# Kernel tuning notes

Measured on AMD Instinct MI355X. Metric: run time of the kernel, lower is better.

The kernel has to match this reference:

```python
import jax, jax.numpy as jnp
import numpy as np

D_MODEL = 1024
N_HEAD = 16
HEAD_DIM = D_MODEL // N_HEAD
D_FF = int(D_MODEL * 4.0)
B, T = 2, 2048


def rms_norm(x, eps=1e-6):
    return x * jax.lax.rsqrt(jnp.mean(jnp.square(x), axis=-1, keepdims=True) + eps)


def rope_tables(T, head_dim):
    # half-truncated RoPE: first quarter of dims get real freqs, next quarter zeros
    angular_freq = (1.0 / 1024.0) ** jnp.linspace(0.0, 1.0, head_dim // 4, dtype=jnp.float32)
    angular_freq = jnp.concatenate([angular_freq, jnp.zeros(head_dim // 4, jnp.float32)])
    theta = jnp.arange(T, dtype=jnp.float32)[:, None] * angular_freq[None, :]  # [T, head_dim//2]
    return jnp.cos(theta), jnp.sin(theta)


def apply_rope(x, cos, sin):
    # x: [B, H, T, D]; cos/sin: [T, D//2]
    x1, x2 = jnp.split(x.astype(jnp.float32), 2, axis=-1)
    c = cos[None, None]
    s = sin[None, None]
    y1 = x1 * c + x2 * s
    y2 = -x1 * s + x2 * c
    return jnp.concatenate([y1, y2], axis=-1).astype(x.dtype)


def setup_inputs() -> dict:
    key = jax.random.key(0)
    ks = jax.random.split(key, 10)
    x = jax.random.normal(ks[0], (B, T, D_MODEL), jnp.float32)
    block_mask = jnp.tril(jnp.ones((T, T), jnp.bool_))  # causal
    sc = 1.0 / np.sqrt(D_MODEL)
    Wqkv = jax.random.normal(ks[1], (D_MODEL, 3 * D_MODEL), jnp.float32) * sc
    bqkv = jnp.zeros((3 * D_MODEL,), jnp.float32)
    Wo = jax.random.normal(ks[2], (D_MODEL, D_MODEL), jnp.float32) * sc
    bo = jnp.zeros((D_MODEL,), jnp.float32)
    W1 = jax.random.normal(ks[3], (D_MODEL, D_FF), jnp.float32) * sc
    b1 = jnp.zeros((D_FF,), jnp.float32)
    W2 = jax.random.normal(ks[4], (D_FF, D_MODEL), jnp.float32) * (1.0 / np.sqrt(D_FF))
    b2 = jnp.zeros((D_MODEL,), jnp.float32)
    return {"x": x, "block_mask": block_mask, "Wqkv": Wqkv, "bqkv": bqkv,
            "Wo": Wo, "bo": bo, "W1": W1, "b1": b1, "W2": W2, "b2": b2}


def reference(x, block_mask, Wqkv, bqkv, Wo, bo, W1, b1, W2, b2):
    Bq, Tq, D = x.shape
    cos, sin = rope_tables(Tq, HEAD_DIM)

    def attn(h):
        qkv = h @ Wqkv + bqkv  # [B, T, 3D]
        qkv = qkv.reshape(Bq, Tq, 3, N_HEAD, HEAD_DIM)
        qkv = jnp.transpose(qkv, (2, 0, 3, 1, 4))  # [3, B, H, T, d]
        q, k, v = qkv[0], qkv[1], qkv[2]
        q, k = rms_norm(q), rms_norm(k)
        q, k = apply_rope(q, cos, sin), apply_rope(k, cos, sin)
        scores = jnp.einsum('bhtd,bhsd->bhts', q, k) / np.sqrt(HEAD_DIM)
        scores = jnp.where(block_mask[None, None], scores, jnp.float32(-1e30))
        p = jax.nn.softmax(scores, axis=-1)
        o = jnp.einsum('bhts,bhsd->bhtd', p, v)
        o = jnp.transpose(o, (0, 2, 1, 3)).reshape(Bq, Tq, D)
        return o @ Wo + bo

    def mlp(h):
        return jax.nn.gelu(h @ W1 + b1) @ W2 + b2

    x = x + attn(rms_norm(x))
    x = x + mlp(rms_norm(x))
    return x
```

## Files before the change

### kernel.cpp

```cpp
#include <hip/hip_runtime.h>
#include <hip/hip_bf16.h>


typedef __attribute__((ext_vector_type(8))) short short8;
typedef __attribute__((ext_vector_type(4))) float f32x4;
typedef __attribute__((ext_vector_type(4))) unsigned short u16x4;
typedef __attribute__((ext_vector_type(8))) unsigned short u16x8;

#define MROWS 4096
#define DMODEL 1024
#define DFF 4096
#define NH 16
#define HD 64
#define SEQ 2048

static __device__ __forceinline__ unsigned short f2bf(float f) {
    union { __hip_bfloat16 b; unsigned short u; } cv;
    cv.b = __float2bfloat16(f);
    return cv.u;
}

static __device__ __forceinline__ void gload_lds16(const void* g, void* l) {
    __builtin_amdgcn_global_load_lds(
        (const __attribute__((address_space(1))) unsigned int*)g,
        (__attribute__((address_space(3))) unsigned int*)l, 16, 0, 0);
}

static __device__ __forceinline__ int xcd_swizzle(int id, int nwg) {
    const int nx = 8;
    const int q = nwg / nx, r = nwg % nx;
    const int xcd = id % nx, loc = id / nx;
    return (xcd < r ? xcd * (q + 1) : r * (q + 1) + (xcd - r) * q) + loc;
}

__global__ void cast_transpose(const float* __restrict__ W,
                               unsigned short* __restrict__ Wt, int K, int N) {
    __shared__ float tile[32][33];
    const int tx = threadIdx.x & 31;
    const int ty = threadIdx.x >> 5;
    const int n0 = blockIdx.x * 32, k0 = blockIdx.y * 32;
#pragma unroll
    for (int i = 0; i < 4; ++i) {
        int kk = ty + i * 8;
        tile[kk][tx] = W[(long)(k0 + kk) * N + n0 + tx];
    }
    __syncthreads();
#pragma unroll
    for (int i = 0; i < 4; ++i) {
        int nn = ty + i * 8;
        Wt[(long)(n0 + nn) * K + k0 + tx] = f2bf(tile[tx][nn]);
    }
}

__global__ void rope_table(float* __restrict__ cosT, float* __restrict__ sinT) {
    const int t = blockIdx.x, j = threadIdx.x;
    float th = (j < 16) ? (float)t * exp2f(-(10.0f / 15.0f) * (float)j) : 0.0f;
    cosT[t * 32 + j] = cosf(th);
    sinT[t * 32 + j] = sinf(th);
}

__global__ void rmsnorm_cast(const float* __restrict__ xin,
                             unsigned short* __restrict__ hout) {
    const int row = blockIdx.x;
    const float4 v = ((const float4*)(xin + (long)row * DMODEL))[threadIdx.x];
    float ss = v.x * v.x + v.y * v.y + v.z * v.z + v.w * v.w;
#pragma unroll
    for (int m = 32; m >= 1; m >>= 1) ss += __shfl_xor(ss, m);
    __shared__ float part[4];
    if ((threadIdx.x & 63) == 0) part[threadIdx.x >> 6] = ss;
    __syncthreads();
    const float tot = part[0] + part[1] + part[2] + part[3];
    const float sc = rsqrtf(tot * (1.0f / (float)DMODEL) + 1e-6f);
    ushort4 o;
    o.x = f2bf(v.x * sc); o.y = f2bf(v.y * sc);
    o.z = f2bf(v.z * sc); o.w = f2bf(v.w * sc);
    ((ushort4*)hout)[(long)row * (DMODEL / 4) + threadIdx.x] = o;
}

template <int EPI, int BN, int BK>
__launch_bounds__(256)
__global__ void gemm_bt(const short* __restrict__ A, const short* __restrict__ Bt,
                        const float* __restrict__ bias, const float* __restrict__ res,
                        float* __restrict__ outF, unsigned short* __restrict__ outB,
                        int N, int K) {
    constexpr int NF = BN / 32;
    constexpr int CPR = BK / 8;
    __shared__ short As[2][128 * BK];
    __shared__ short Bs[2][BN * BK];
    const int tid = threadIdx.x;
    const int lane = tid & 63, w = tid >> 6;
    const int wr = w >> 1, wc = w & 1;
    const int l16 = lane & 15, lhi = lane >> 4;

    const int nwg = gridDim.x * gridDim.y;
    int id = xcd_swizzle(blockIdx.y * gridDim.x + blockIdx.x, nwg);
    const int bx = id % gridDim.x, by = id / gridDim.x;
    const long rowA0 = (long)by * 128;
    const long rowB0 = (long)bx * BN;

    const f32x4 fz = {0.f, 0.f, 0.f, 0.f};
    f32x4 acc[4][NF];
#pragma unroll
    for (int m = 0; m < 4; ++m)
#pragma unroll
        for (int n = 0; n < NF; ++n) acc[m][n] = fz;

    auto stage = [&](int kt, int b) {
        const int k0 = kt * BK;
#pragma unroll
        for (int it = 0; it < BK / 16; ++it) {
            const int c = it * 256 + tid;
            const int r = c / CPR, col = (c % CPR) * 8;
            gload_lds16(A + (rowA0 + r) * K + k0 + col, (char*)As[b] + c * 16);
        }
#pragma unroll
        for (int it = 0; it < (BN * BK) / 2048; ++it) {
            const int c = it * 256 + tid;
            const int r = c / CPR, col = (c % CPR) * 8;
            gload_lds16(Bt + (rowB0 + r) * K + k0 + col, (char*)Bs[b] + c * 16);
        }
    };
    auto compute = [&](int b) {
#pragma unroll
        for (int kk = 0; kk < BK / 32; ++kk) {
            short8 af[4], bf[NF];
#pragma unroll
            for (int m = 0; m < 4; ++m)
                af[m] = *(const short8*)(&As[b][0] + (wr * 64 + m * 16 + l16) * BK + kk * 32 + lhi * 8);
#pragma unroll
            for (int n = 0; n < NF; ++n)
                bf[n] = *(const short8*)(&Bs[b][0] + (wc * (BN / 2) + n * 16 + l16) * BK + kk * 32 + lhi * 8);
#pragma unroll
            for (int m = 0; m < 4; ++m)
#pragma unroll
                for (int n = 0; n < NF; ++n)
                    acc[m][n] = __builtin_amdgcn_mfma_f32_16x16x32_bf16(
                        af[m], bf[n], acc[m][n], 0, 0, 0);
        }
    };

    const int ktiles = K / BK;
    stage(0, 0);
    __syncthreads();
    int cur = 0;
    for (int kt = 0; kt < ktiles; ++kt) {
        if (kt + 1 < ktiles) stage(kt + 1, cur ^ 1);
        compute(cur);
        __syncthreads();
        cur ^= 1;
    }

#pragma unroll
    for (int m = 0; m < 4; ++m) {
        const long r0 = rowA0 + wr * 64 + m * 16 + lhi * 4;
#pragma unroll
        for (int n = 0; n < NF; ++n) {
            const long cc = rowB0 + wc * (BN / 2) + n * 16 + l16;
            const float bv = bias[cc];
#pragma unroll
            for (int j = 0; j < 4; ++j) {
                const long idx = (r0 + j) * N + cc;
                float v = acc[m][n][j] + bv;
                if (EPI == 1) v += res[idx];
                if (EPI == 2) {
                    float g = 0.5f * v *
                        (1.0f + tanhf(0.7978845608028654f * (v + 0.044715f * v * v * v)));
                    outB[idx] = f2bf(g);
                } else {
                    outF[idx] = v;
                }
            }
        }
    }
}

__global__ void qkv_post(const float* __restrict__ qkv, const float* __restrict__ cosT,
                         const float* __restrict__ sinT, unsigned short* __restrict__ Qo,
                         unsigned short* __restrict__ Ko) {
    const int lane = threadIdx.x & 63;
    const int g = blockIdx.x * 4 + (threadIdx.x >> 6);
    const int row = g >> 4, h = g & 15;
    const int b = row >> 11, t = row & 2047;
    const float* base = qkv + (long)row * 3072 + h * 64;
    float q = base[lane];
    float k = base[1024 + lane];
    float sq = q * q, sk = k * k;
#pragma unroll
    for (int m = 32; m >= 1; m >>= 1) {
        sq += __shfl_xor(sq, m);
        sk += __shfl_xor(sk, m);
    }
    q *= rsqrtf(sq * (1.0f / 64.0f) + 1e-6f);
    k *= rsqrtf(sk * (1.0f / 64.0f) + 1e-6f);
    const int j = lane & 31;
    const float c = cosT[t * 32 + j], s = sinT[t * 32 + j];
    const float q2 = __shfl_xor(q, 32), k2 = __shfl_xor(k, 32);
    const float sgn = (lane < 32) ? 1.0f : -1.0f;
    const float qr = q * c + sgn * q2 * s;
    const float kr = k * c + sgn * k2 * s;
    const long o = ((long)(b * 16 + h) * SEQ + t) * 64 + lane;
    Qo[o] = f2bf(qr * 0.125f);
    Ko[o] = f2bf(kr);
}

__global__ void transpose_v(const float* __restrict__ qkv,
                            unsigned short* __restrict__ Vt) {
    __shared__ float tile[64][65];
    const int tid = threadIdx.x;
    const int bh = blockIdx.x, tt = blockIdx.y;
    const int b = bh >> 4, h = bh & 15;
    const int tr = tid >> 2, c0 = (tid & 3) * 16;
    const float* src = qkv + ((long)(b * SEQ + tt * 64 + tr)) * 3072 + 2048 + h * 64 + c0;
#pragma unroll
    for (int i = 0; i < 4; ++i) {
        float4 v = ((const float4*)src)[i];
        tile[tr][c0 + i * 4 + 0] = v.x;
        tile[tr][c0 + i * 4 + 1] = v.y;
        tile[tr][c0 + i * 4 + 2] = v.z;
        tile[tr][c0 + i * 4 + 3] = v.w;
    }
    __syncthreads();
    const int d = tid >> 2, t0 = (tid & 3) * 16;
    unsigned short* dst = Vt + ((long)bh * 64 + d) * SEQ + tt * 64 + t0;
#pragma unroll
    for (int half = 0; half < 2; ++half) {
        u16x8 o;
#pragma unroll
        for (int e = 0; e < 8; ++e) o[e] = f2bf(tile[t0 + half * 8 + e][d]);
        *(u16x8*)(dst + half * 8) = o;
    }
}

__launch_bounds__(256)
__global__ void attn_fwd(const short* __restrict__ Qg, const short* __restrict__ Kg,
                         const short* __restrict__ Vtg, unsigned short* __restrict__ Og) {
    __shared__ short Ks[2][64 * 64];
    __shared__ short Vs[2][64 * 64];
    __shared__ char Ps[4][2048];
    const int tid = threadIdx.x, lane = tid & 63, w = tid >> 6;
    const int l16 = lane & 15, lhi = lane >> 4;
    const int id = xcd_swizzle(blockIdx.y * gridDim.x + blockIdx.x, 512);
    const int bh = id >> 4;
    const int ip = id & 15;
    const int bb = bh >> 4, hh = bh & 15;
    const long base_q = (long)bh * (SEQ * 64);
    char* Pw = &Ps[w][0];
    const int swz = (l16 & 7) << 4;
    const f32x4 fz = {0.f, 0.f, 0.f, 0.f};

#pragma unroll 1
    for (int rep = 0; rep < 2; ++rep) {
        const int qt = rep ? ip : 31 - ip;
        short8 aq0, aq1;
        {
            const short* Qp = Qg + base_q + (long)(qt * 64 + w * 16) * 64;
            aq0 = *(const short8*)(Qp + l16 * 64 + lhi * 8);
            aq1 = *(const short8*)(Qp + l16 * 64 + 32 + lhi * 8);
        }
        float mrow = -1e30f, lrow = 0.f;
        f32x4 oacc[4];
#pragma unroll
        for (int n = 0; n < 4; ++n) oacc[n] = fz;

        auto stage = [&](int kt, int b) {
            const short* Kp = Kg + base_q + (long)kt * 64 * 64;
            const short* Vp = Vtg + base_q + (long)kt * 64;
#pragma unroll
            for (int it = 0; it < 2; ++it) {
                const int c = it * 256 + tid;
                const int r = c >> 3;
                const int col = ((c & 7) ^ (r & 7)) << 3;
                gload_lds16(Kp + r * 64 + col, (char*)&Ks[b][0] + c * 16);
                gload_lds16(Vp + (long)r * SEQ + col, (char*)&Vs[b][0] + c * 16);
            }
        };

        stage(0, 0);
        __syncthreads();
        int cur = 0;
        for (int kt = 0; kt <= qt; ++kt) {
            if (kt < qt) stage(kt + 1, cur ^ 1);
            const short* KsC = &Ks[cur][0];
            const short* VsC = &Vs[cur][0];

            f32x4 s[4];
            __builtin_amdgcn_s_setprio(1);
#pragma unroll
            for (int n = 0; n < 4; ++n) {
                const int kr = n * 16 + l16;
                short8 bk0 = *(const short8*)(KsC + kr * 64 + ((lhi ^ (kr & 7)) << 3));
                short8 bk1 = *(const short8*)(KsC + kr * 64 + (((lhi + 4) ^ (kr & 7)) << 3));
                f32x4 z = fz;
                z = __builtin_amdgcn_mfma_f32_16x16x32_bf16(bk0, aq0, z, 0, 0, 0);
                s[n] = __builtin_amdgcn_mfma_f32_16x16x32_bf16(bk1, aq1, z, 0, 0, 0);
            }
            __builtin_amdgcn_s_setprio(0);
            if (kt == qt) {
#pragma unroll
                for (int n = 0; n < 4; ++n)
#pragma unroll
                    for (int j = 0; j < 4; ++j)
                        if (n * 16 + lhi * 4 + j > w * 16 + l16) s[n][j] = -1e30f;
            }

            float pm = s[0][0];
#pragma unroll
            for (int n = 0; n < 4; ++n)
#pragma unroll
                for (int j = 0; j < 4; ++j) pm = fmaxf(pm, s[n][j]);
            pm = fmaxf(pm, __shfl_xor(pm, 16));
            pm = fmaxf(pm, __shfl_xor(pm, 32));
            if (!__all(pm <= mrow + 8.f)) {
                const float newm = fmaxf(mrow, pm);
                const float sc = __expf(mrow - newm);
                mrow = newm;
                lrow *= sc;
#pragma unroll
                for (int j = 0; j < 4; ++j) {
                    const float scj = __shfl(sc, lhi * 4 + j);
#pragma unroll
                    for (int n = 0; n < 4; ++n) oacc[n][j] *= scj;
                }
            }
            float ps = 0.f;
#pragma unroll
            for (int n = 0; n < 4; ++n)
#pragma unroll
                for (int j = 0; j < 4; ++j) {
                    const float p = __expf(s[n][j] - mrow);
                    s[n][j] = p;
                    ps += p;
                }
            ps += __shfl_xor(ps, 16);
            ps += __shfl_xor(ps, 32);
            lrow += ps;

#pragma unroll
            for (int n = 0; n < 4; ++n) {
                u16x4 pk;
                pk[0] = f2bf(s[n][0]);
                pk[1] = f2bf(s[n][1]);
                pk[2] = f2bf(s[n][2]);
                pk[3] = f2bf(s[n][3]);
                *(u16x4*)(Pw + ((l16 * 128 + n * 32 + lhi * 8) ^ swz)) = pk;
            }

            __builtin_amdgcn_s_setprio(1);
#pragma unroll
            for (int ks = 0; ks < 2; ++ks) {
                short8 pa = *(const short8*)(Pw + ((l16 * 128 + ks * 64 + lhi * 16) ^ swz));
#pragma unroll
                for (int n = 0; n < 4; ++n) {
                    const int dr = n * 16 + l16;
                    short8 vb = *(const short8*)(VsC + dr * 64 + ((((ks << 2) + lhi) ^ (dr & 7)) << 3));
                    oacc[n] = __builtin_amdgcn_mfma_f32_16x16x32_bf16(pa, vb, oacc[n], 0, 0, 0);
                }
            }
            __builtin_amdgcn_s_setprio(0);
            __syncthreads();
            cur ^= 1;
        }

#pragma unroll
        for (int j = 0; j < 4; ++j) {
            const float lr = __shfl(lrow, lhi * 4 + j);
            const int qrow = qt * 64 + w * 16 + lhi * 4 + j;
            const long orow = (long)bb * SEQ + qrow;
#pragma unroll
            for (int n = 0; n < 4; ++n)
                Og[orow * DMODEL + hh * 64 + n * 16 + l16] = f2bf(oacc[n][j] / lr);
        }
    }
}

extern "C" void kernel_launch(void* const* d_in, const int* in_sizes, int n_in,
                              void* d_out, int out_size, void* d_ws, size_t ws_size,
                              hipStream_t stream) {
    const float* x    = (const float*)d_in[0];
    const float* Wqkv = (const float*)d_in[2];
    const float* bqkv = (const float*)d_in[3];
    const float* Wo   = (const float*)d_in[4];
    const float* bo   = (const float*)d_in[5];
    const float* W1   = (const float*)d_in[6];
    const float* b1   = (const float*)d_in[7];
    const float* W2   = (const float*)d_in[8];
    const float* b2   = (const float*)d_in[9];
    float* out = (float*)d_out;

    char* ws = (char*)d_ws;
    auto alloc = [&](size_t b) {
        char* p = ws;
        ws += (b + 255) & ~(size_t)255;
        return p;
    };
    short* WqkvT = (short*)alloc(3072ull * 1024 * 2);
    short* WoT   = (short*)alloc(1024ull * 1024 * 2);
    short* W1T   = (short*)alloc(4096ull * 1024 * 2);
    short* W2T   = (short*)alloc(1024ull * 4096 * 2);
    float* cosT  = (float*)alloc(2048ull * 32 * 4);
    float* sinT  = (float*)alloc(2048ull * 32 * 4);
    short* hbuf  = (short*)alloc((size_t)MROWS * DMODEL * 2);
    short* Qb    = (short*)alloc(32ull * SEQ * 64 * 2);
    short* Kb    = (short*)alloc(32ull * SEQ * 64 * 2);
    short* Vtb   = (short*)alloc(32ull * 64 * SEQ * 2);
    short* Ob    = (short*)alloc((size_t)MROWS * DMODEL * 2);
    float* x1    = (float*)alloc((size_t)MROWS * DMODEL * 4);
    char*  big   = alloc((size_t)MROWS * 3072 * 4);
    float* qkv   = (float*)big;
    unsigned short* act = (unsigned short*)big;

    cast_transpose<<<dim3(96, 32), 256, 0, stream>>>(Wqkv, (unsigned short*)WqkvT, 1024, 3072);
    cast_transpose<<<dim3(32, 32), 256, 0, stream>>>(Wo, (unsigned short*)WoT, 1024, 1024);
    cast_transpose<<<dim3(128, 32), 256, 0, stream>>>(W1, (unsigned short*)W1T, 1024, 4096);
    cast_transpose<<<dim3(32, 128), 256, 0, stream>>>(W2, (unsigned short*)W2T, 4096, 1024);
    rope_table<<<2048, 32, 0, stream>>>(cosT, sinT);
    rmsnorm_cast<<<MROWS, 256, 0, stream>>>(x, (unsigned short*)hbuf);
    gemm_bt<0, 128, 32><<<dim3(24, 32), 256, 0, stream>>>(hbuf, WqkvT, bqkv, nullptr, qkv, nullptr, 3072, 1024);
    qkv_post<<<16384, 256, 0, stream>>>(qkv, cosT, sinT,
                                        (unsigned short*)Qb, (unsigned short*)Kb);
    transpose_v<<<dim3(32, 32), 256, 0, stream>>>(qkv, (unsigned short*)Vtb);
    attn_fwd<<<dim3(16, 32), 256, 0, stream>>>(Qb, Kb, Vtb, (unsigned short*)Ob);
    gemm_bt<1, 64, 64><<<dim3(16, 32), 256, 0, stream>>>(Ob, WoT, bo, x, x1, nullptr, 1024, 1024);
    rmsnorm_cast<<<MROWS, 256, 0, stream>>>(x1, (unsigned short*)hbuf);
    gemm_bt<2, 128, 32><<<dim3(32, 32), 256, 0, stream>>>(hbuf, W1T, b1, nullptr, nullptr, act, 4096, 1024);
    gemm_bt<1, 64, 64><<<dim3(16, 32), 256, 0, stream>>>((const short*)act, W2T, b2, x1, out, nullptr, 1024, 4096);
}
```

Before: 412.8 us.

## Add 256x256-tile 512-thread GEMM with 4-stage LDS pipeline for QKV and FFN1

Adds a new GEMM kernel that uses 256x256 output tiles, 8 waves per block and a four-buffer direct-to-LDS prefetch pipeline with swizzled LDS layout and explicit vmcnt waits. It replaces the 128-wide gemm_bt for the QKV projection and the first MLP matmul, aiming for more data reuse per loaded tile and better latency hiding. The larger tiles give far fewer workgroups (192 and 256), which may underfill the 256 CUs, and the 64 KB of LDS plus large accumulator arrays per block may limit occupancy.

```diff
diff --git a/kernel.cpp b/kernel.cpp
--- a/kernel.cpp
+++ b/kernel.cpp
@@ -75,6 +75,108 @@
     o.x = f2bf(v.x * sc); o.y = f2bf(v.y * sc);
     o.z = f2bf(v.z * sc); o.w = f2bf(v.w * sc);
     ((ushort4*)hout)[(long)row * (DMODEL / 4) + threadIdx.x] = o;
+}
+
+template <int EPI>
+__launch_bounds__(512, 2)
+__global__ void gemm256(const short* __restrict__ A, const short* __restrict__ Bt,
+                        const float* __restrict__ bias,
+                        float* __restrict__ outF, unsigned short* __restrict__ outB,
+                        int N, int K) {
+    __shared__ __align__(16) short As[4][128 * 64];
+    __shared__ __align__(16) short Bs[4][128 * 64];
+    const int tid = threadIdx.x;
+    const int lane = tid & 63, w = tid >> 6;
+    const int wr = w >> 2, wc = w & 3;
+    const int l16 = lane & 15, lhi = lane >> 4;
+
+    const int nwg = gridDim.x * gridDim.y;
+    int id = xcd_swizzle(blockIdx.y * gridDim.x + blockIdx.x, nwg);
+    const int bx = id % gridDim.x, by = id / gridDim.x;
+    const long rowA0 = (long)by * 256;
+    const long rowB0 = (long)bx * 256;
+
+    const f32x4 fz = {0.f, 0.f, 0.f, 0.f};
+    f32x4 acc[8][4];
+#pragma unroll
+    for (int m = 0; m < 8; ++m)
+#pragma unroll
+        for (int n = 0; n < 4; ++n) acc[m][n] = fz;
+
+    auto stage = [&](int kt, int b) {
+        const int k0 = kt << 5;
+#pragma unroll
+        for (int pass = 0; pass < 2; ++pass) {
+            const int c = pass * 512 + tid;
+            const int line = c >> 3, pch = c & 7;
+            const int lch = pch ^ (line & 7);
+            const int row = ((lch >> 2) << 7) + line;
+            const int kc = (lch & 3) << 3;
+            gload_lds16(A + (rowA0 + row) * K + k0 + kc, (char*)&As[b][0] + c * 16);
+            gload_lds16(Bt + (rowB0 + row) * K + k0 + kc, (char*)&Bs[b][0] + c * 16);
+        }
+    };
+    auto compute = [&](int b) {
+        const short* Ab = &As[b][0];
+        const short* Bb = &Bs[b][0];
+        short8 af[8], bf[4];
+#pragma unroll
+        for (int m = 0; m < 8; ++m) {
+            const int line = m * 16 + l16;
+            const int pch = ((wr << 2) + lhi) ^ (line & 7);
+            af[m] = *(const short8*)(Ab + line * 64 + pch * 8);
+        }
+#pragma unroll
+        for (int n = 0; n < 4; ++n) {
+            const int row = wc * 64 + n * 16 + l16;
+            const int line = row & 127;
+            const int pch = (((row >> 7) << 2) + lhi) ^ (line & 7);
+            bf[n] = *(const short8*)(Bb + line * 64 + pch * 8);
+        }
+#pragma unroll
+        for (int m = 0; m < 8; ++m)
+#pragma unroll
+            for (int n = 0; n < 4; ++n)
+                acc[m][n] = __builtin_amdgcn_mfma_f32_16x16x32_bf16(
+                    af[m], bf[n], acc[m][n], 0, 0, 0);
+    };
+
+    const int ktiles = K >> 5;
+    stage(0, 0);
+    stage(1, 1);
+    stage(2, 2);
+    for (int t = 0; t < ktiles; ++t) {
+        const int rem = ktiles - 1 - t;
+        if (rem >= 2)      asm volatile("s_waitcnt vmcnt(8)" ::: "memory");
+        else if (rem == 1) asm volatile("s_waitcnt vmcnt(4)" ::: "memory");
+        else               asm volatile("s_waitcnt vmcnt(0)" ::: "memory");
+        __builtin_amdgcn_s_barrier();
+        __builtin_amdgcn_sched_barrier(0);
+        if (t + 3 < ktiles) stage(t + 3, (t + 3) & 3);
+        compute(t & 3);
+    }
+
+#pragma unroll
+    for (int m = 0; m < 8; ++m) {
+        const long r0 = rowA0 + wr * 128 + m * 16 + lhi * 4;
+#pragma unroll
+        for (int n = 0; n < 4; ++n) {
+            const long cc = rowB0 + wc * 64 + n * 16 + l16;
+            const float bv = bias[cc];
+#pragma unroll
+            for (int j = 0; j < 4; ++j) {
+                const long idx = (r0 + j) * N + cc;
+                float v = acc[m][n][j] + bv;
+                if (EPI == 2) {
+                    float g = 0.5f * v *
+                        (1.0f + tanhf(0.7978845608028654f * (v + 0.044715f * v * v * v)));
+                    outB[idx] = f2bf(g);
+                } else {
+                    outF[idx] = v;
+                }
+            }
+        }
+    }
 }
 
 template <int EPI, int BN, int BK>
@@ -415,13 +517,13 @@
     cast_transpose<<<dim3(32, 128), 256, 0, stream>>>(W2, (unsigned short*)W2T, 4096, 1024);
     rope_table<<<2048, 32, 0, stream>>>(cosT, sinT);
     rmsnorm_cast<<<MROWS, 256, 0, stream>>>(x, (unsigned short*)hbuf);
-    gemm_bt<0, 128, 32><<<dim3(24, 32), 256, 0, stream>>>(hbuf, WqkvT, bqkv, nullptr, qkv, nullptr, 3072, 1024);
+    gemm256<0><<<dim3(12, 16), 512, 0, stream>>>(hbuf, WqkvT, bqkv, qkv, nullptr, 3072, 1024);
     qkv_post<<<16384, 256, 0, stream>>>(qkv, cosT, sinT,
                                         (unsigned short*)Qb, (unsigned short*)Kb);
     transpose_v<<<dim3(32, 32), 256, 0, stream>>>(qkv, (unsigned short*)Vtb);
     attn_fwd<<<dim3(16, 32), 256, 0, stream>>>(Qb, Kb, Vtb, (unsigned short*)Ob);
     gemm_bt<1, 64, 64><<<dim3(16, 32), 256, 0, stream>>>(Ob, WoT, bo, x, x1, nullptr, 1024, 1024);
     rmsnorm_cast<<<MROWS, 256, 0, stream>>>(x1, (unsigned short*)hbuf);
-    gemm_bt<2, 128, 32><<<dim3(32, 32), 256, 0, stream>>>(hbuf, W1T, b1, nullptr, nullptr, act, 4096, 1024);
+    gemm256<2><<<dim3(16, 16), 512, 0, stream>>>(hbuf, W1T, b1, nullptr, act, 4096, 1024);
     gemm_bt<1, 64, 64><<<dim3(16, 32), 256, 0, stream>>>((const short*)act, W2T, b2, x1, out, nullptr, 1024, 4096);
 }
```

Result: no change. 419.0 us (+1.5%).
